# Kernel tuning notes

Hardware: AMD Instinct MI355X
Metric: run time of the kernel (lower is better)

## Reference

```python
import jax, jax.numpy as jnp
import numpy as np

MAX_DELAY = 128
INPUT = 64
HIDDEN = 128
HALF = HIDDEN // 2
OUT = 64
B = 32
T = 128
OUT_LEN = 64


def setup_inputs() -> dict:
    key = jax.random.key(0)
    ks = jax.random.split(key, 10)
    w = lambda k, sh: (jax.random.normal(k, sh, jnp.float32) * 0.05)
    return {
        "x": jax.random.normal(ks[0], (B, T, INPUT), jnp.float32),
        "lengths": jax.random.randint(ks[1], (B,), 0, T, jnp.int32),
        "out_lengths": OUT_LEN,
        "Wm": w(ks[2], (INPUT + HIDDEN, HIDDEN)), "bm": jnp.zeros((HIDDEN,), jnp.float32),
        "W1": w(ks[3], (HIDDEN, HALF)), "b1": jnp.zeros((HALF,), jnp.float32),
        "W2": w(ks[4], (HALF, 2 * HIDDEN)), "b2": jnp.zeros((2 * HIDDEN,), jnp.float32),
        "Wo": w(ks[5], (HIDDEN, OUT)), "bo": jnp.zeros((OUT,), jnp.float32),
    }


def reference(x, lengths, out_lengths, Wm, bm, W1, b1, W2, b2, Wo, bo):
    # index_tensor: (1, 1, max_delay) in [0, 1)
    index = (jnp.arange(MAX_DELAY, dtype=x.dtype) / MAX_DELAY)[None, None, :]

    def tau_gen(msg):  # msg: (B, H)
        h = jax.nn.relu(msg @ W1 + b1)
        tg = jax.nn.sigmoid(h @ W2 + b2)  # (B, 2H)
        return tg[:, :HIDDEN], tg[:, HIDDEN:]

    def update_buffer(buffer, msg, tau, mem_i):
        # shift left, zero-pad at the end
        new_buf = jnp.pad(buffer[:, :, 1:], ((0, 0), (0, 0), (0, 1)))
        iw = mem_i[..., None] * (1.0 - jnp.abs(tau[..., None] - index)) ** 2  # (B,H,D)
        return (1.0 - iw) * new_buf + iw * msg[..., None]

    masks = (jnp.arange(T) < lengths[:, None]).astype(x.dtype)  # (B, T)

    def enc_step(buffer, inp):
        x_t, mask = inp  # (B, I), (B,)
        m = mask[:, None]  # (B, 1)
        msg = m * jnp.tanh(jnp.concatenate([x_t, buffer[:, :, 0]], axis=-1) @ Wm + bm)
        tau, mem_i = tau_gen(msg)
        new_buf = update_buffer(buffer, msg, tau, mem_i)
        buffer = jnp.where(m[..., None] > 0, new_buf, buffer)
        return buffer, None

    buffer0 = jnp.zeros((B, HIDDEN, MAX_DELAY), x.dtype)
    buffer, _ = jax.lax.scan(enc_step, buffer0, (x.transpose(1, 0, 2), masks.T))

    x0 = jnp.zeros((B, INPUT), x.dtype)

    def dec_step(buffer, _):
        msg = jnp.tanh(jnp.concatenate([x0, buffer[:, :, 0]], axis=-1) @ Wm + bm)
        tau, mem_i = tau_gen(msg)
        buffer = update_buffer(buffer, msg, tau, mem_i)
        return buffer, msg @ Wo + bo

    _, outs = jax.lax.scan(dec_step, buffer, None, length=out_lengths)
    return outs.transpose(1, 0, 2)  # (B, out_lengths, OUT)
```

## Files before the change

### kernel.cpp

```cpp
#include <hip/hip_runtime.h>
#include <math.h>

typedef __attribute__((ext_vector_type(2))) float f32x2;
typedef __attribute__((ext_vector_type(4))) float f32x4;

#define MAX_DELAY 128
#define INPUT 64
#define HIDDEN 128
#define HALF 64
#define OUT 64
#define BATCH 32
#define T 128
#define OUT_LEN 64
#define NTHR 512

static __device__ __forceinline__ f32x2 splat2(float v) { f32x2 r; r.x = v; r.y = v; return r; }
static __device__ __forceinline__ f32x4 splat4(float v) { f32x4 r; r.x = v; r.y = v; r.z = v; r.w = v; return r; }

template <int CTRL>
static __device__ __forceinline__ float dpp_movf(float v) {
    return __int_as_float(__builtin_amdgcn_update_dpp(
        0, __float_as_int(v), CTRL, 0xF, 0xF, true));
}
#define DPP_XOR1 0xB1
#define DPP_XOR2 0x4E
#define DPP_ROT1 0x39
#define DPP_MIR8 0x141

__global__ __launch_bounds__(NTHR, 2)
void delayrnn_kernel(
    const float* __restrict__ x,
    const int*   __restrict__ lengths,
    const float* __restrict__ Wm,
    const float* __restrict__ bm,
    const float* __restrict__ W1,
    const float* __restrict__ b1,
    const float* __restrict__ W2,
    const float* __restrict__ b2,
    const float* __restrict__ Wo,
    const float* __restrict__ bo,
    float* __restrict__ out)
{
    const int b   = blockIdx.x;
    const int tid = threadIdx.x;
    const int len = lengths[b];
    const int total = len + OUT_LEN;

    const int h  = tid >> 2, q  = tid & 3;
    const int qq = q & 1,    qh = q >> 1;
    const int k1 = tid >> 3, r1 = tid & 7;
    const int co = tid >> 3, ro = tid & 7;
    const int c2 = h + 128 * qh;

    f32x4 wm4[12];
#pragma unroll
    for (int j = 0; j < 12; ++j) {
        wm4[j].x = Wm[(q * 48 + 4 * j    ) * HIDDEN + h];
        wm4[j].y = Wm[(q * 48 + 4 * j + 1) * HIDDEN + h];
        wm4[j].z = Wm[(q * 48 + 4 * j + 2) * HIDDEN + h];
        wm4[j].w = Wm[(q * 48 + 4 * j + 3) * HIDDEN + h];
    }
    f32x4 w14[4];
#pragma unroll
    for (int j = 0; j < 4; ++j) {
        w14[j].x = W1[(r1 * 16 + 4 * j    ) * HALF + k1];
        w14[j].y = W1[(r1 * 16 + 4 * j + 1) * HALF + k1];
        w14[j].z = W1[(r1 * 16 + 4 * j + 2) * HALF + k1];
        w14[j].w = W1[(r1 * 16 + 4 * j + 3) * HALF + k1];
    }
    f32x4 w24[8];
#pragma unroll
    for (int j = 0; j < 8; ++j) {
        w24[j].x = W2[(qq * 32 + 4 * j    ) * (2 * HIDDEN) + c2];
        w24[j].y = W2[(qq * 32 + 4 * j + 1) * (2 * HIDDEN) + c2];
        w24[j].z = W2[(qq * 32 + 4 * j + 2) * (2 * HIDDEN) + c2];
        w24[j].w = W2[(qq * 32 + 4 * j + 3) * (2 * HIDDEN) + c2];
    }
    f32x4 wo4[4];
#pragma unroll
    for (int m = 0; m < 4; ++m) {
        wo4[m].x = Wo[(ro * 16 + 4 * m    ) * OUT + co];
        wo4[m].y = Wo[(ro * 16 + 4 * m + 1) * OUT + co];
        wo4[m].z = Wo[(ro * 16 + 4 * m + 2) * OUT + co];
        wo4[m].w = Wo[(ro * 16 + 4 * m + 3) * OUT + co];
    }
    const float bm_r = bm[h];
    const float b1_r = b1[k1];
    const float b2_r = b2[c2];
    const float bo_r = bo[co];

    f32x2 buf2[16];
#pragma unroll
    for (int d = 0; d < 16; ++d) { buf2[d].x = 0.f; buf2[d].y = 0.f; }

    __shared__ f32x4 s_x4[T * INPUT / 4];
    __shared__ f32x4 s_v4[48];
    __shared__ f32x4 s_msg4[48];
    __shared__ float s_h1[HALF];

    {
        const f32x4* xg4 = (const f32x4*)x;
        for (int idx = tid; idx < T * INPUT / 4; idx += NTHR)
            s_x4[idx] = xg4[b * (T * INPUT / 4) + idx];
        if (tid < 16) s_v4[tid] = (0 < len) ? xg4[b * (T * INPUT / 4) + tid] : splat4(0.f);
        if (tid >= 16 && tid < 48) s_v4[tid] = splat4(0.f);
    }
    __syncthreads();

    const float ivb = (float)q * 0.25f;
    float msg_p = 0.f, tau_p = 0.f, mem_p = 0.f;

    for (int i = 0; i < total; ++i) {
        const f32x4* v4 = s_v4 + q * 12;
        f32x4 a0 = splat4(0.f), a1 = splat4(0.f), a2 = splat4(0.f), a3 = splat4(0.f);
#pragma unroll
        for (int j = 0; j < 12; j += 4) {
            a0 += wm4[j]     * v4[j];
            a1 += wm4[j + 1] * v4[j + 1];
            a2 += wm4[j + 2] * v4[j + 2];
            a3 += wm4[j + 3] * v4[j + 3];
        }

        {
            float tail_in = dpp_movf<DPP_ROT1>(buf2[0].x);
            if (q == 3) tail_in = 0.f;
            const float taup = tau_p - ivb;
            f32x2 t2; t2.x = taup; t2.y = taup - (1.f / MAX_DELAY);
            const f32x2 st2  = splat2(-2.f / MAX_DELAY);
            const f32x2 mem2 = splat2(mem_p);
            const f32x2 m2m  = splat2(-2.f * mem_p);
            const f32x2 msg2 = splat2(msg_p);
#pragma unroll
            for (int d = 0; d < 16; ++d) {
                f32x2 nb;
                nb.x = buf2[d].y;
                nb.y = (d < 15) ? buf2[d + 1].x : tail_in;
                f32x2 a  = __builtin_elementwise_max(t2, -t2);
                f32x2 f1 = a * mem2 + m2m;
                f32x2 iw = a * f1 + mem2;
                f32x2 dd = msg2 - nb;
                buf2[d] = iw * dd + nb;
                t2 = t2 + st2;
            }
        }

        f32x4 s4 = (a0 + a1) + (a2 + a3);
        float p = (s4.x + s4.z) + (s4.y + s4.w);
        p += dpp_movf<DPP_XOR1>(p);
        p += dpp_movf<DPP_XOR2>(p);
        const float z  = p + bm_r;
        const float e2 = __expf(2.f * z);
        const float msg = 1.f - 2.f * __builtin_amdgcn_rcpf(e2 + 1.f);
        if (q == 0) ((float*)s_msg4)[h + ((h >> 4) << 3)] = msg;
        msg_p = msg;
        __syncthreads();

        {
            const f32x4* m4 = (const f32x4*)((const float*)s_msg4 + r1 * 24);
            f32x4 cA = w14[0] * m4[0] + w14[2] * m4[2];
            f32x4 cB = w14[1] * m4[1] + w14[3] * m4[3];
            f32x4 cc = cA + cB;
            float p1 = (cc.x + cc.z) + (cc.y + cc.w);
            p1 += dpp_movf<DPP_XOR1>(p1);
            p1 += dpp_movf<DPP_XOR2>(p1);
            p1 += dpp_movf<DPP_MIR8>(p1);
            if (r1 == 0) s_h1[k1] = fmaxf(p1 + b1_r, 0.f);
        }

        if (tid < 16) {
            const int nx = i + 1;
            f32x4 nv = splat4(0.f);
            if (nx < len) nv = s_x4[nx * 16 + tid];
            s_v4[tid] = nv;
        }

        if (i >= len) {
            const f32x4* mo4 = s_msg4 + ro * 6;
            f32x4 oA = wo4[0] * mo4[0] + wo4[2] * mo4[2];
            f32x4 oB = wo4[1] * mo4[1] + wo4[3] * mo4[3];
            f32x4 oo = oA + oB;
            float po = (oo.x + oo.z) + (oo.y + oo.w);
            po += dpp_movf<DPP_XOR1>(po);
            po += dpp_movf<DPP_XOR2>(po);
            po += dpp_movf<DPP_MIR8>(po);
            if (ro == 0) out[(b * OUT_LEN + (i - len)) * OUT + co] = po + bo_r;
        }
        __syncthreads();

        {
            const f32x4* hh4 = (const f32x4*)(s_h1 + (qq << 5));
            f32x4 tA = w24[0] * hh4[0] + w24[2] * hh4[2] + w24[4] * hh4[4] + w24[6] * hh4[6];
            f32x4 tB = w24[1] * hh4[1] + w24[3] * hh4[3] + w24[5] * hh4[5] + w24[7] * hh4[7];
            f32x4 tt = tA + tB;
            float pt = (tt.x + tt.z) + (tt.y + tt.w);
            pt += dpp_movf<DPP_XOR1>(pt);
            const float own = __builtin_amdgcn_rcpf(1.f + __expf(-(pt + b2_r)));
            const float oth = dpp_movf<DPP_XOR2>(own);
            const float tau_r = qh ? oth : own;
            const float mem_r = qh ? own : oth;
            tau_p = tau_r; mem_p = mem_r;

            const float nb0 = buf2[0].y;
            const float iw0 = tau_r * (tau_r * mem_r - 2.f * mem_r) + mem_r;
            const float head = iw0 * (msg_p - nb0) + nb0;
            if (q == 0) ((float*)s_v4)[INPUT + h] = head;
        }
        __syncthreads();
    }
}

extern "C" void kernel_launch(void* const* d_in, const int* in_sizes, int n_in,
                              void* d_out, int out_size, void* d_ws, size_t ws_size,
                              hipStream_t stream) {
    const float* x       = (const float*)d_in[0];
    const int*   lengths = (const int*)  d_in[1];
    const float* Wm = (const float*)d_in[3];
    const float* bm = (const float*)d_in[4];
    const float* W1 = (const float*)d_in[5];
    const float* b1 = (const float*)d_in[6];
    const float* W2 = (const float*)d_in[7];
    const float* b2 = (const float*)d_in[8];
    const float* Wo = (const float*)d_in[9];
    const float* bo = (const float*)d_in[10];
    float* out = (float*)d_out;

    delayrnn_kernel<<<BATCH, NTHR, 0, stream>>>(
        x, lengths, Wm, bm, W1, b1, W2, b2, Wo, bo, out);
}
```

Measured before the change: 314.3 us.

## Double threads per block and split each hidden unit across eight lanes

The block grows from 512 to 1024 threads, so each hidden unit is handled by 8 lanes instead of 4. Each lane now holds half as much of the delay buffer and half of each weight slice, and the DPP reduction trees get one or two extra stages (MIR8/MIR16, SHL1 in place of ROT1). The aim is to shorten the per-step serial critical path of this latency-bound recurrence by spreading the work. In exchange it adds cross-lane reduction steps and makes the per-step barriers span twice as many waves.

```diff
diff --git a/kernel.cpp b/kernel.cpp
--- a/kernel.cpp
+++ b/kernel.cpp
@@ -12,7 +12,7 @@
 #define BATCH 32
 #define T 128
 #define OUT_LEN 64
-#define NTHR 512
+#define NTHR 1024
 
 static __device__ __forceinline__ f32x2 splat2(float v) { f32x2 r; r.x = v; r.y = v; return r; }
 static __device__ __forceinline__ f32x4 splat4(float v) { f32x4 r; r.x = v; r.y = v; r.z = v; r.w = v; return r; }
@@ -24,10 +24,13 @@
 }
 #define DPP_XOR1 0xB1
 #define DPP_XOR2 0x4E
-#define DPP_ROT1 0x39
 #define DPP_MIR8 0x141
-
-__global__ __launch_bounds__(NTHR, 2)
+#define DPP_MIR16 0x140
+#define DPP_SHL1 0x101
+
+#define PAD8(k) ((k) + (((k) >> 3) << 2))
+
+__global__ __launch_bounds__(NTHR, 4)
 void delayrnn_kernel(
     const float* __restrict__ x,
     const int*   __restrict__ lengths,
@@ -46,57 +49,56 @@
     const int len = lengths[b];
     const int total = len + OUT_LEN;
 
-    const int h  = tid >> 2, q  = tid & 3;
-    const int qq = q & 1,    qh = q >> 1;
-    const int k1 = tid >> 3, r1 = tid & 7;
-    const int co = tid >> 3, ro = tid & 7;
+    const int h  = tid >> 3, r  = tid & 7;
+    const int qh = r >> 2,   kq = r & 3;
+    const int k1 = tid >> 4, r1 = tid & 15;
     const int c2 = h + 128 * qh;
 
-    f32x4 wm4[12];
-#pragma unroll
-    for (int j = 0; j < 12; ++j) {
-        wm4[j].x = Wm[(q * 48 + 4 * j    ) * HIDDEN + h];
-        wm4[j].y = Wm[(q * 48 + 4 * j + 1) * HIDDEN + h];
-        wm4[j].z = Wm[(q * 48 + 4 * j + 2) * HIDDEN + h];
-        wm4[j].w = Wm[(q * 48 + 4 * j + 3) * HIDDEN + h];
-    }
-    f32x4 w14[4];
+    f32x4 wm4[6];
+#pragma unroll
+    for (int j = 0; j < 6; ++j) {
+        wm4[j].x = Wm[(r * 24 + 4 * j    ) * HIDDEN + h];
+        wm4[j].y = Wm[(r * 24 + 4 * j + 1) * HIDDEN + h];
+        wm4[j].z = Wm[(r * 24 + 4 * j + 2) * HIDDEN + h];
+        wm4[j].w = Wm[(r * 24 + 4 * j + 3) * HIDDEN + h];
+    }
+    f32x4 w14[2];
+#pragma unroll
+    for (int j = 0; j < 2; ++j) {
+        w14[j].x = W1[(r1 * 8 + 4 * j    ) * HALF + k1];
+        w14[j].y = W1[(r1 * 8 + 4 * j + 1) * HALF + k1];
+        w14[j].z = W1[(r1 * 8 + 4 * j + 2) * HALF + k1];
+        w14[j].w = W1[(r1 * 8 + 4 * j + 3) * HALF + k1];
+    }
+    f32x4 w24[4];
 #pragma unroll
     for (int j = 0; j < 4; ++j) {
-        w14[j].x = W1[(r1 * 16 + 4 * j    ) * HALF + k1];
-        w14[j].y = W1[(r1 * 16 + 4 * j + 1) * HALF + k1];
-        w14[j].z = W1[(r1 * 16 + 4 * j + 2) * HALF + k1];
-        w14[j].w = W1[(r1 * 16 + 4 * j + 3) * HALF + k1];
-    }
-    f32x4 w24[8];
-#pragma unroll
-    for (int j = 0; j < 8; ++j) {
-        w24[j].x = W2[(qq * 32 + 4 * j    ) * (2 * HIDDEN) + c2];
-        w24[j].y = W2[(qq * 32 + 4 * j + 1) * (2 * HIDDEN) + c2];
-        w24[j].z = W2[(qq * 32 + 4 * j + 2) * (2 * HIDDEN) + c2];
-        w24[j].w = W2[(qq * 32 + 4 * j + 3) * (2 * HIDDEN) + c2];
-    }
-    f32x4 wo4[4];
-#pragma unroll
-    for (int m = 0; m < 4; ++m) {
-        wo4[m].x = Wo[(ro * 16 + 4 * m    ) * OUT + co];
-        wo4[m].y = Wo[(ro * 16 + 4 * m + 1) * OUT + co];
-        wo4[m].z = Wo[(ro * 16 + 4 * m + 2) * OUT + co];
-        wo4[m].w = Wo[(ro * 16 + 4 * m + 3) * OUT + co];
+        w24[j].x = W2[(kq * 16 + 4 * j    ) * (2 * HIDDEN) + c2];
+        w24[j].y = W2[(kq * 16 + 4 * j + 1) * (2 * HIDDEN) + c2];
+        w24[j].z = W2[(kq * 16 + 4 * j + 2) * (2 * HIDDEN) + c2];
+        w24[j].w = W2[(kq * 16 + 4 * j + 3) * (2 * HIDDEN) + c2];
+    }
+    f32x4 wo4[2];
+#pragma unroll
+    for (int m = 0; m < 2; ++m) {
+        wo4[m].x = Wo[(r1 * 8 + 4 * m    ) * OUT + k1];
+        wo4[m].y = Wo[(r1 * 8 + 4 * m + 1) * OUT + k1];
+        wo4[m].z = Wo[(r1 * 8 + 4 * m + 2) * OUT + k1];
+        wo4[m].w = Wo[(r1 * 8 + 4 * m + 3) * OUT + k1];
     }
     const float bm_r = bm[h];
     const float b1_r = b1[k1];
     const float b2_r = b2[c2];
-    const float bo_r = bo[co];
-
-    f32x2 buf2[16];
-#pragma unroll
-    for (int d = 0; d < 16; ++d) { buf2[d].x = 0.f; buf2[d].y = 0.f; }
+    const float bo_r = bo[k1];
+
+    f32x2 buf2[8];
+#pragma unroll
+    for (int d = 0; d < 8; ++d) { buf2[d].x = 0.f; buf2[d].y = 0.f; }
 
     __shared__ f32x4 s_x4[T * INPUT / 4];
     __shared__ f32x4 s_v4[48];
     __shared__ f32x4 s_msg4[48];
-    __shared__ float s_h1[HALF];
+    __shared__ f32x4 s_h14[24];
 
     {
         const f32x4* xg4 = (const f32x4*)x;
@@ -107,23 +109,21 @@
     }
     __syncthreads();
 
-    const float ivb = (float)q * 0.25f;
+    const float ivb = (float)r * 0.125f;
     float msg_p = 0.f, tau_p = 0.f, mem_p = 0.f;
 
     for (int i = 0; i < total; ++i) {
-        const f32x4* v4 = s_v4 + q * 12;
-        f32x4 a0 = splat4(0.f), a1 = splat4(0.f), a2 = splat4(0.f), a3 = splat4(0.f);
-#pragma unroll
-        for (int j = 0; j < 12; j += 4) {
-            a0 += wm4[j]     * v4[j];
-            a1 += wm4[j + 1] * v4[j + 1];
-            a2 += wm4[j + 2] * v4[j + 2];
-            a3 += wm4[j + 3] * v4[j + 3];
-        }
+        const f32x4* v4 = s_v4 + r * 6;
+        f32x4 a0 = wm4[0] * v4[0];
+        f32x4 a1 = wm4[1] * v4[1];
+        f32x4 a2 = wm4[2] * v4[2];
+        a0 += wm4[3] * v4[3];
+        a1 += wm4[4] * v4[4];
+        a2 += wm4[5] * v4[5];
 
         {
-            float tail_in = dpp_movf<DPP_ROT1>(buf2[0].x);
-            if (q == 3) tail_in = 0.f;
+            float tail_in = dpp_movf<DPP_SHL1>(buf2[0].x);
+            if (r == 7) tail_in = 0.f;
             const float taup = tau_p - ivb;
             f32x2 t2; t2.x = taup; t2.y = taup - (1.f / MAX_DELAY);
             const f32x2 st2  = splat2(-2.f / MAX_DELAY);
@@ -131,10 +131,10 @@
             const f32x2 m2m  = splat2(-2.f * mem_p);
             const f32x2 msg2 = splat2(msg_p);
 #pragma unroll
-            for (int d = 0; d < 16; ++d) {
+            for (int d = 0; d < 8; ++d) {
                 f32x2 nb;
                 nb.x = buf2[d].y;
-                nb.y = (d < 15) ? buf2[d + 1].x : tail_in;
+                nb.y = (d < 7) ? buf2[d + 1].x : tail_in;
                 f32x2 a  = __builtin_elementwise_max(t2, -t2);
                 f32x2 f1 = a * mem2 + m2m;
                 f32x2 iw = a * f1 + mem2;
@@ -144,27 +144,27 @@
             }
         }
 
-        f32x4 s4 = (a0 + a1) + (a2 + a3);
+        f32x4 s4 = a0 + a1 + a2;
         float p = (s4.x + s4.z) + (s4.y + s4.w);
         p += dpp_movf<DPP_XOR1>(p);
         p += dpp_movf<DPP_XOR2>(p);
+        p += dpp_movf<DPP_MIR8>(p);
         const float z  = p + bm_r;
         const float e2 = __expf(2.f * z);
         const float msg = 1.f - 2.f * __builtin_amdgcn_rcpf(e2 + 1.f);
-        if (q == 0) ((float*)s_msg4)[h + ((h >> 4) << 3)] = msg;
+        if (r == 0) ((float*)s_msg4)[PAD8(h)] = msg;
         msg_p = msg;
         __syncthreads();
 
         {
-            const f32x4* m4 = (const f32x4*)((const float*)s_msg4 + r1 * 24);
-            f32x4 cA = w14[0] * m4[0] + w14[2] * m4[2];
-            f32x4 cB = w14[1] * m4[1] + w14[3] * m4[3];
-            f32x4 cc = cA + cB;
+            const f32x4* m4 = (const f32x4*)((const float*)s_msg4 + r1 * 12);
+            f32x4 cc = w14[0] * m4[0] + w14[1] * m4[1];
             float p1 = (cc.x + cc.z) + (cc.y + cc.w);
             p1 += dpp_movf<DPP_XOR1>(p1);
             p1 += dpp_movf<DPP_XOR2>(p1);
             p1 += dpp_movf<DPP_MIR8>(p1);
-            if (r1 == 0) s_h1[k1] = fmaxf(p1 + b1_r, 0.f);
+            p1 += dpp_movf<DPP_MIR16>(p1);
+            if (r1 == 0) ((float*)s_h14)[PAD8(k1)] = fmaxf(p1 + b1_r, 0.f);
         }
 
         if (tid < 16) {
@@ -175,27 +175,29 @@
         }
 
         if (i >= len) {
-            const f32x4* mo4 = s_msg4 + ro * 6;
-            f32x4 oA = wo4[0] * mo4[0] + wo4[2] * mo4[2];
-            f32x4 oB = wo4[1] * mo4[1] + wo4[3] * mo4[3];
-            f32x4 oo = oA + oB;
+            const f32x4* mo4 = (const f32x4*)((const float*)s_msg4 + r1 * 12);
+            f32x4 oo = wo4[0] * mo4[0] + wo4[1] * mo4[1];
             float po = (oo.x + oo.z) + (oo.y + oo.w);
             po += dpp_movf<DPP_XOR1>(po);
             po += dpp_movf<DPP_XOR2>(po);
             po += dpp_movf<DPP_MIR8>(po);
-            if (ro == 0) out[(b * OUT_LEN + (i - len)) * OUT + co] = po + bo_r;
+            po += dpp_movf<DPP_MIR16>(po);
+            if (r1 == 0) out[(b * OUT_LEN + (i - len)) * OUT + k1] = po + bo_r;
         }
         __syncthreads();
 
         {
-            const f32x4* hh4 = (const f32x4*)(s_h1 + (qq << 5));
-            f32x4 tA = w24[0] * hh4[0] + w24[2] * hh4[2] + w24[4] * hh4[4] + w24[6] * hh4[6];
-            f32x4 tB = w24[1] * hh4[1] + w24[3] * hh4[3] + w24[5] * hh4[5] + w24[7] * hh4[7];
-            f32x4 tt = tA + tB;
+            const float* hb = (const float*)s_h14 + kq * 24;
+            const f32x4 h0 = *(const f32x4*)(hb);
+            const f32x4 h1v = *(const f32x4*)(hb + 4);
+            const f32x4 h2 = *(const f32x4*)(hb + 12);
+            const f32x4 h3 = *(const f32x4*)(hb + 16);
+            f32x4 tt = (w24[0] * h0 + w24[2] * h2) + (w24[1] * h1v + w24[3] * h3);
             float pt = (tt.x + tt.z) + (tt.y + tt.w);
             pt += dpp_movf<DPP_XOR1>(pt);
+            pt += dpp_movf<DPP_XOR2>(pt);
             const float own = __builtin_amdgcn_rcpf(1.f + __expf(-(pt + b2_r)));
-            const float oth = dpp_movf<DPP_XOR2>(own);
+            const float oth = dpp_movf<DPP_MIR8>(own);
             const float tau_r = qh ? oth : own;
             const float mem_r = qh ? own : oth;
             tau_p = tau_r; mem_p = mem_r;
@@ -203,7 +205,7 @@
             const float nb0 = buf2[0].y;
             const float iw0 = tau_r * (tau_r * mem_r - 2.f * mem_r) + mem_r;
             const float head = iw0 * (msg_p - nb0) + nb0;
-            if (q == 0) ((float*)s_v4)[INPUT + h] = head;
+            if (r == 0) ((float*)s_v4)[INPUT + h] = head;
         }
         __syncthreads();
     }
```

Result: slower. 353.8 us (+12.5%).

## Precompute next-step input projection off critical path and stage outputs in LDS

Applied to the files above, without the earlier changes.

Splits the Wm matvec into an input part and a hidden part. The next timestep's x·Wm partial is computed while the previous step finishes, so the per-step critical path only covers the 128-element hidden dot. The hidden vector gets its own padded LDS layout to avoid bank conflicts. Decoder outputs are buffered in shared memory and written to global memory in one coalesced burst at the end. This adds 16KB of LDS per block and some extra registers, which could reduce occupancy.

```diff
diff --git a/kernel.cpp b/kernel.cpp
--- a/kernel.cpp
+++ b/kernel.cpp
@@ -26,6 +26,9 @@
 #define DPP_XOR2 0x4E
 #define DPP_ROT1 0x39
 #define DPP_MIR8 0x141
+
+#define PAD16(k) ((k) + (((k) >> 4) << 3))
+#define PADH(k)  ((k) + (((k) >> 5) << 2))
 
 __global__ __launch_bounds__(NTHR, 2)
 void delayrnn_kernel(
@@ -52,13 +55,21 @@
     const int co = tid >> 3, ro = tid & 7;
     const int c2 = h + 128 * qh;
 
-    f32x4 wm4[12];
-#pragma unroll
-    for (int j = 0; j < 12; ++j) {
-        wm4[j].x = Wm[(q * 48 + 4 * j    ) * HIDDEN + h];
-        wm4[j].y = Wm[(q * 48 + 4 * j + 1) * HIDDEN + h];
-        wm4[j].z = Wm[(q * 48 + 4 * j + 2) * HIDDEN + h];
-        wm4[j].w = Wm[(q * 48 + 4 * j + 3) * HIDDEN + h];
+    f32x4 wmh[8];
+#pragma unroll
+    for (int j = 0; j < 8; ++j) {
+        wmh[j].x = Wm[(64 + q * 32 + 4 * j    ) * HIDDEN + h];
+        wmh[j].y = Wm[(64 + q * 32 + 4 * j + 1) * HIDDEN + h];
+        wmh[j].z = Wm[(64 + q * 32 + 4 * j + 2) * HIDDEN + h];
+        wmh[j].w = Wm[(64 + q * 32 + 4 * j + 3) * HIDDEN + h];
+    }
+    f32x4 wmx[4];
+#pragma unroll
+    for (int j = 0; j < 4; ++j) {
+        wmx[j].x = Wm[(q * 16 + 4 * j    ) * HIDDEN + h];
+        wmx[j].y = Wm[(q * 16 + 4 * j + 1) * HIDDEN + h];
+        wmx[j].z = Wm[(q * 16 + 4 * j + 2) * HIDDEN + h];
+        wmx[j].w = Wm[(q * 16 + 4 * j + 3) * HIDDEN + h];
     }
     f32x4 w14[4];
 #pragma unroll
@@ -94,32 +105,35 @@
     for (int d = 0; d < 16; ++d) { buf2[d].x = 0.f; buf2[d].y = 0.f; }
 
     __shared__ f32x4 s_x4[T * INPUT / 4];
-    __shared__ f32x4 s_v4[48];
+    __shared__ float s_vh[140];
     __shared__ f32x4 s_msg4[48];
     __shared__ float s_h1[HALF];
+    __shared__ f32x4 s_out4[OUT_LEN * OUT / 4];
 
     {
         const f32x4* xg4 = (const f32x4*)x;
         for (int idx = tid; idx < T * INPUT / 4; idx += NTHR)
             s_x4[idx] = xg4[b * (T * INPUT / 4) + idx];
-        if (tid < 16) s_v4[tid] = (0 < len) ? xg4[b * (T * INPUT / 4) + tid] : splat4(0.f);
-        if (tid >= 16 && tid < 48) s_v4[tid] = splat4(0.f);
+        if (tid < 35) ((f32x4*)s_vh)[tid] = splat4(0.f);
     }
     __syncthreads();
+
+    float px = 0.f;
+    if (0 < len) {
+        const f32x4* xs = s_x4 + q * 4;
+        f32x4 t = (wmx[0] * xs[0] + wmx[2] * xs[2]) + (wmx[1] * xs[1] + wmx[3] * xs[3]);
+        px = (t.x + t.z) + (t.y + t.w);
+    }
 
     const float ivb = (float)q * 0.25f;
     float msg_p = 0.f, tau_p = 0.f, mem_p = 0.f;
 
     for (int i = 0; i < total; ++i) {
-        const f32x4* v4 = s_v4 + q * 12;
-        f32x4 a0 = splat4(0.f), a1 = splat4(0.f), a2 = splat4(0.f), a3 = splat4(0.f);
-#pragma unroll
-        for (int j = 0; j < 12; j += 4) {
-            a0 += wm4[j]     * v4[j];
-            a1 += wm4[j + 1] * v4[j + 1];
-            a2 += wm4[j + 2] * v4[j + 2];
-            a3 += wm4[j + 3] * v4[j + 3];
-        }
+        const f32x4* v4 = (const f32x4*)(s_vh + q * 36);
+        f32x4 a0 = wmh[0] * v4[0] + wmh[4] * v4[4];
+        f32x4 a1 = wmh[1] * v4[1] + wmh[5] * v4[5];
+        f32x4 a2 = wmh[2] * v4[2] + wmh[6] * v4[6];
+        f32x4 a3 = wmh[3] * v4[3] + wmh[7] * v4[7];
 
         {
             float tail_in = dpp_movf<DPP_ROT1>(buf2[0].x);
@@ -145,13 +159,13 @@
         }
 
         f32x4 s4 = (a0 + a1) + (a2 + a3);
-        float p = (s4.x + s4.z) + (s4.y + s4.w);
+        float p = (s4.x + s4.z) + (s4.y + s4.w) + px;
         p += dpp_movf<DPP_XOR1>(p);
         p += dpp_movf<DPP_XOR2>(p);
         const float z  = p + bm_r;
         const float e2 = __expf(2.f * z);
         const float msg = 1.f - 2.f * __builtin_amdgcn_rcpf(e2 + 1.f);
-        if (q == 0) ((float*)s_msg4)[h + ((h >> 4) << 3)] = msg;
+        if (q == 0) ((float*)s_msg4)[PAD16(h)] = msg;
         msg_p = msg;
         __syncthreads();
 
@@ -167,15 +181,15 @@
             if (r1 == 0) s_h1[k1] = fmaxf(p1 + b1_r, 0.f);
         }
 
-        if (tid < 16) {
-            const int nx = i + 1;
-            f32x4 nv = splat4(0.f);
-            if (nx < len) nv = s_x4[nx * 16 + tid];
-            s_v4[tid] = nv;
+        px = 0.f;
+        if (i + 1 < len) {
+            const f32x4* xs = s_x4 + (i + 1) * 16 + q * 4;
+            f32x4 t = (wmx[0] * xs[0] + wmx[2] * xs[2]) + (wmx[1] * xs[1] + wmx[3] * xs[3]);
+            px = (t.x + t.z) + (t.y + t.w);
         }
 
         if (i >= len) {
-            const f32x4* mo4 = s_msg4 + ro * 6;
+            const f32x4* mo4 = (const f32x4*)((const float*)s_msg4 + ro * 24);
             f32x4 oA = wo4[0] * mo4[0] + wo4[2] * mo4[2];
             f32x4 oB = wo4[1] * mo4[1] + wo4[3] * mo4[3];
             f32x4 oo = oA + oB;
@@ -183,7 +197,7 @@
             po += dpp_movf<DPP_XOR1>(po);
             po += dpp_movf<DPP_XOR2>(po);
             po += dpp_movf<DPP_MIR8>(po);
-            if (ro == 0) out[(b * OUT_LEN + (i - len)) * OUT + co] = po + bo_r;
+            if (ro == 0) ((float*)s_out4)[(i - len) * OUT + co] = po + bo_r;
         }
         __syncthreads();
 
@@ -203,9 +217,15 @@
             const float nb0 = buf2[0].y;
             const float iw0 = tau_r * (tau_r * mem_r - 2.f * mem_r) + mem_r;
             const float head = iw0 * (msg_p - nb0) + nb0;
-            if (q == 0) ((float*)s_v4)[INPUT + h] = head;
+            if (q == 0) s_vh[PADH(h)] = head;
         }
         __syncthreads();
+    }
+
+    {
+        f32x4* og4 = (f32x4*)(out + b * OUT_LEN * OUT);
+        og4[tid]        = s_out4[tid];
+        og4[tid + NTHR] = s_out4[tid + NTHR];
     }
 }
 
```

New measurement: 311.2 us. About the same (-1.0%).
